# Kernel optimization log

Measured on AMD Instinct MI355X. Metric: run time of the kernel, lower is better.

The kernel has to match this reference:

```python
import jax, jax.numpy as jnp
import numpy as np

B, C, H = 2, 32, 64  # batch, concat channels, cube side (H==W==D required by attaxis reshapes)
Ch = C // 2


def _conv3d(x, w, b, pad):
    # conv3d block = Conv3d + bias + ReLU (n=1 conv block)
    y = jax.lax.conv_general_dilated(x, w, (1, 1, 1), [(p, p) for p in pad],
                                     dimension_numbers=('NCDHW', 'OIDHW', 'NCDHW'))
    return jax.nn.relu(y + b[None, :, None, None, None])


def setup_inputs():
    key = jax.random.key(0)
    ks = jax.random.split(key, 16)
    w = lambda k, s: jax.random.normal(k, s, dtype=jnp.float32) * 0.05
    z = lambda n: jnp.zeros((n,), jnp.float32)
    return {
        'x1': jax.random.normal(ks[0], (B, Ch, H, H, H), jnp.float32),
        'x2': jax.random.normal(ks[1], (B, Ch, H, H, H), jnp.float32),
        'w_red': w(ks[2], (1, C, 3, 3, 3)), 'b_red': z(1),
        'w_cx': w(ks[3], (1, 1, 1, 1, H)), 'b_cx': z(1),
        'w_cy': w(ks[4], (1, 1, 1, H, 1)), 'b_cy': z(1),
        'w_cz': w(ks[5], (1, 1, H, 1, 1)), 'b_cz': z(1),
        'w_sp1': w(ks[6], (1, 1, 1, 1, 1)), 'b_sp1': z(1),
        'w_sp3': w(ks[7], (1, 1, 3, 3, 3)), 'b_sp3': z(1),
        'w_sp5a': w(ks[8], (1, 1, 3, 3, 3)), 'b_sp5a': z(1),
        'w_sp5b': w(ks[9], (1, 1, 3, 3, 3)), 'b_sp5b': z(1),
        'w_fus': w(ks[10], (C, 1, 3, 3, 3)), 'b_fus': z(C),
        'w_c1': w(ks[11], (Ch, Ch, 3, 3, 3)), 'b_c1': z(Ch),
        'w_c2': w(ks[12], (Ch, Ch, 3, 3, 3)), 'b_c2': z(Ch),
    }


def _kernal(x, w_cx, b_cx, w_cy, b_cy, w_cz, b_cz,
            w_sp1, b_sp1, w_sp3, b_sp3, w_sp5a, b_sp5a, w_sp5b, b_sp5b):
    b, c, h, ww, d = x.shape
    # xyzaxis: axis-collapsing convs, then attaxis attention over S = h*w tokens
    q = _conv3d(x, w_cx, b_cx, (0, 0, 0))                        # [b,1,h,w,1]
    k = jnp.swapaxes(_conv3d(x, w_cy, b_cy, (0, 0, 0)), 3, 4)    # [b,1,h,d,1]
    v = jnp.swapaxes(_conv3d(x, w_cz, b_cz, (0, 0, 0)), 2, 4)    # [b,1,d,w,1]
    S = h * ww
    Q = q.reshape(b, S, 1)
    K = k.reshape(b, S, 1)
    V = v.reshape(b, S, 1)
    qk = jax.nn.softmax(jnp.einsum('bsc,btc->bst', Q, K), axis=-1)  # [b,S,S]
    xyz = jnp.einsum('bst,btc->bsc', qk, V).reshape(b, 1, h, ww, 1)
    # multi-branch convs + full-tensor att(sp1, sp3, sp5)
    sp1 = _conv3d(x, w_sp1, b_sp1, (0, 0, 0))
    sp3 = _conv3d(x, w_sp3, b_sp3, (1, 1, 1))
    sp5 = _conv3d(_conv3d(x, w_sp5a, b_sp5a, (1, 1, 1)), w_sp5b, b_sp5b, (1, 1, 1))
    attn = jnp.matmul(jax.nn.softmax(jnp.matmul(sp1, sp3), axis=-1), sp5)
    return xyz + attn + x  # xyz broadcasts over last dim


def reference(x1, x2, w_red, b_red, w_cx, b_cx, w_cy, b_cy, w_cz, b_cz,
              w_sp1, b_sp1, w_sp3, b_sp3, w_sp5a, b_sp5a, w_sp5b, b_sp5b,
              w_fus, b_fus, w_c1, b_c1, w_c2, b_c2):
    x = jnp.concatenate([x1, x2], axis=1)                 # [B,C,H,H,H]
    hx = _conv3d(x, w_red, b_red, (1, 1, 1))              # DenseSP.reducePool -> 1 channel
    hx = _kernal(hx, w_cx, b_cx, w_cy, b_cy, w_cz, b_cz,
                 w_sp1, b_sp1, w_sp3, b_sp3, w_sp5a, b_sp5a, w_sp5b, b_sp5b)
    sp = jax.nn.sigmoid(_conv3d(hx, w_fus, b_fus, (1, 1, 1)) + x)  # DenseSP output
    x = sp * x + x
    c = x.shape[1] // 2
    y1 = _conv3d(x[:, :c] + x1, w_c1, b_c1, (1, 1, 1))
    y2 = _conv3d(x[:, c:] + x2, w_c2, b_c2, (1, 1, 1))
    return (y1, y2)
```

## Files before the change

kernel.cpp:

```cpp
#include <hip/hip_runtime.h>

#define DEVFN static __device__ __forceinline__

constexpr int HHH = 262144;
constexpr int HH  = 4096;
constexpr int SP  = 20;

typedef __attribute__((ext_vector_type(8))) short short8;
typedef __attribute__((ext_vector_type(4))) float f32x4;

#define OFF_HX   ((size_t)0)
#define OFF_SP3  (OFF_HX   + 2*(size_t)HHH)
#define OFF_SP5A (OFF_SP3  + 2*(size_t)HHH)
#define OFF_SP5B (OFF_SP5A + 2*(size_t)HHH)
#define OFF_HXO  (OFF_SP5B + 2*(size_t)HHH)
#define OFF_Q    (OFF_HXO  + 2*(size_t)HHH)
#define OFF_K    (OFF_Q    + 2*(size_t)HH)
#define OFF_V    (OFF_K    + 2*(size_t)HH)
#define OFF_XYZ  (OFF_V    + 2*(size_t)HH)
#define OFF_KM   (OFF_XYZ  + 2*(size_t)HH)
#define OFF_Z    (OFF_KM   + 16)
#define OFF_WPRE (OFF_Z    + 32*(size_t)HHH)

DEVFN unsigned short f2bf(float f)
{
    unsigned u = __builtin_bit_cast(unsigned, f);
    u += 0x7fffu + ((u >> 16) & 1u);
    return (unsigned short)(u >> 16);
}

DEVFN void stage20(const float* __restrict__ src, float* __restrict__ tile,
                   int z0, int y0, int x0, int tid)
{
    for (int i = tid; i < 1800; i += 256) {
        int lz = i / 180;
        int r  = i - lz * 180;
        int ly = r / 18;
        int lx = r - ly * 18;
        int gz = z0 - 1 + lz, gy = y0 - 1 + ly, gx = x0 - 1 + lx;
        float v = 0.f;
        if ((unsigned)(gz | gy | gx) < 64u)
            v = src[(gz * 64 + gy) * 64 + gx];
        tile[(lz * 10 + ly) * SP + lx] = v;
    }
}

DEVFN void loadnb(const float* __restrict__ tile, int tz, int ty, int txg,
                  float4* pa, float2* pb)
{
#pragma unroll
    for (int dz = 0; dz < 3; ++dz) {
#pragma unroll
        for (int dy = 0; dy < 3; ++dy) {
            const float* row = &tile[((tz + dz) * 10 + (ty + dy)) * SP + txg * 4];
            pa[dz * 3 + dy] = *(const float4*)row;
            pb[dz * 3 + dy] = *(const float2*)(row + 4);
        }
    }
}

DEVFN float4 conv27r(const float4* pa, const float2* pb,
                     const float* __restrict__ wc, float4 acc)
{
#pragma unroll
    for (int t = 0; t < 9; ++t) {
        float w0 = wc[3 * t], w1 = wc[3 * t + 1], w2 = wc[3 * t + 2];
        float4 p = pa[t];
        float2 q = pb[t];
        acc.x = fmaf(p.x, w0, fmaf(p.y, w1, fmaf(p.z, w2, acc.x)));
        acc.y = fmaf(p.y, w0, fmaf(p.z, w1, fmaf(p.w, w2, acc.y)));
        acc.z = fmaf(p.z, w0, fmaf(p.w, w1, fmaf(q.x, w2, acc.z)));
        acc.w = fmaf(p.w, w0, fmaf(q.x, w1, fmaf(q.y, w2, acc.w)));
    }
    return acc;
}

__global__ __launch_bounds__(256) void k_wprep(
    const float* __restrict__ w1, const float* __restrict__ w2,
    unsigned short* __restrict__ wpre)
{
    int item = blockIdx.x * 256 + threadIdx.x;
    if (item >= 1792) return;
    int half = item / 896;
    int rem  = item - half * 896;
    int t = rem >> 6, lane = rem & 63;
    const float* w = half ? w2 : w1;
    int co = lane & 15, g = lane >> 4;
    int cihalf = g & 1, tapsel = g >> 1;
    int tap = 2 * t + tapsel;
    unsigned v[4] = {0u, 0u, 0u, 0u};
    if (tap < 27) {
#pragma unroll
        for (int p = 0; p < 4; ++p) {
            unsigned short lo = f2bf(w[(co * 16 + cihalf * 8 + 2 * p) * 27 + tap]);
            unsigned short hi = f2bf(w[(co * 16 + cihalf * 8 + 2 * p + 1) * 27 + tap]);
            v[p] = (unsigned)lo | ((unsigned)hi << 16);
        }
    }
    uint4 pk = {v[0], v[1], v[2], v[3]};
    ((uint4*)wpre)[item] = pk;
}

__global__ __launch_bounds__(256) void k_conv_red32(
    const float* __restrict__ x1, const float* __restrict__ x2,
    const float* __restrict__ w, const float* __restrict__ bias,
    float* __restrict__ hx)
{
    __shared__ __align__(16) float buf[3][2000];
    const int tid = threadIdx.x;
    const int tz = tid >> 5, ty = (tid >> 2) & 7, txg = tid & 3;
    const int bz = blockIdx.z;
    const int b = bz >> 3, z0 = (bz & 7) * 8;
    const int y0 = blockIdx.y * 8, x0 = blockIdx.x * 16;

    int gofs[8], lidx[8];
    bool inb[8], act[8];
#pragma unroll
    for (int k = 0; k < 8; ++k) {
        int i = tid + k * 256;
        act[k] = (i < 1800);
        inb[k] = false; gofs[k] = 0; lidx[k] = 0;
        if (act[k]) {
            int lz = i / 180, r = i - lz * 180, ly = r / 18, lx = r - ly * 18;
            lidx[k] = (lz * 10 + ly) * SP + lx;
            int gz = z0 - 1 + lz, gy = y0 - 1 + ly, gx = x0 - 1 + lx;
            if ((unsigned)(gz | gy | gx) < 64u) {
                inb[k] = true;
                gofs[k] = (gz * 64 + gy) * 64 + gx;
            }
        }
    }

#define LOADCH(c, rdst)                                                         \
    {                                                                           \
        const float* s_ = ((c) < 16 ? x1 : x2) + (size_t)(b * 16 + ((c) & 15)) * HHH; \
        _Pragma("unroll")                                                       \
        for (int k = 0; k < 8; ++k) rdst[k] = (act[k] && inb[k]) ? s_[gofs[k]] : 0.f; \
    }
#define STORECH(buf_, rsrc)                                                     \
    {                                                                           \
        _Pragma("unroll")                                                       \
        for (int k = 0; k < 8; ++k) if (act[k]) (buf_)[lidx[k]] = rsrc[k];      \
    }

    float rcur[8], rnext[8];
    LOADCH(0, rcur);
    STORECH(buf[0], rcur);
    LOADCH(1, rcur);
    __syncthreads();

    float4 acc = {0.f, 0.f, 0.f, 0.f};
    int cur = 0;
    for (int c = 0; c < 32; ++c) {
        if (c + 2 < 32) LOADCH(c + 2, rnext);
        const float* wc = w + c * 27;
        const float* tb = buf[cur];
#pragma unroll
        for (int dz = 0; dz < 3; ++dz) {
#pragma unroll
            for (int dy = 0; dy < 3; ++dy) {
                const float* row = &tb[((tz + dz) * 10 + (ty + dy)) * SP + txg * 4];
                float4 p = *(const float4*)row;
                float2 q = *(const float2*)(row + 4);
                const float* wr = wc + (dz * 3 + dy) * 3;
                float w0 = wr[0], w1 = wr[1], w2 = wr[2];
                acc.x = fmaf(p.x, w0, fmaf(p.y, w1, fmaf(p.z, w2, acc.x)));
                acc.y = fmaf(p.y, w0, fmaf(p.z, w1, fmaf(p.w, w2, acc.y)));
                acc.z = fmaf(p.z, w0, fmaf(p.w, w1, fmaf(q.x, w2, acc.z)));
                acc.w = fmaf(p.w, w0, fmaf(q.x, w1, fmaf(q.y, w2, acc.w)));
            }
        }
        int nxt = cur == 2 ? 0 : cur + 1;
        if (c + 1 < 32) {
            STORECH(buf[nxt], rcur);
#pragma unroll
            for (int k = 0; k < 8; ++k) rcur[k] = rnext[k];
        }
        cur = nxt;
        __syncthreads();
    }
#undef LOADCH
#undef STORECH

    float bv = bias[0];
    float4 o = {fmaxf(acc.x + bv, 0.f), fmaxf(acc.y + bv, 0.f),
                fmaxf(acc.z + bv, 0.f), fmaxf(acc.w + bv, 0.f)};
    size_t oidx = (size_t)b * HHH + ((size_t)(z0 + tz) * 64 + (y0 + ty)) * 64 + (x0 + txg * 4);
    *(float4*)&hx[oidx] = o;
}

__global__ __launch_bounds__(256) void k_conv1ch(
    const float* __restrict__ in, const float* __restrict__ w,
    const float* __restrict__ bias, float* __restrict__ outp)
{
    __shared__ __align__(16) float tile[2000];
    const int tid = threadIdx.x;
    const int tz = tid >> 5, ty = (tid >> 2) & 7, txg = tid & 3;
    const int b  = blockIdx.z >> 3;
    const int z0 = (blockIdx.z & 7) * 8, y0 = blockIdx.y * 8, x0 = blockIdx.x * 16;

    stage20(in + (size_t)b * HHH, tile, z0, y0, x0, tid);
    __syncthreads();
    float4 pa[9]; float2 pb[9];
    loadnb(tile, tz, ty, txg, pa, pb);
    float4 acc = {0.f, 0.f, 0.f, 0.f};
    acc = conv27r(pa, pb, w, acc);
    float bv = bias[0];
    float4 o = {fmaxf(acc.x + bv, 0.f), fmaxf(acc.y + bv, 0.f),
                fmaxf(acc.z + bv, 0.f), fmaxf(acc.w + bv, 0.f)};
    size_t oidx = (size_t)b * HHH + ((size_t)(z0 + tz) * 64 + (y0 + ty)) * 64 + (x0 + txg * 4);
    *(float4*)&outp[oidx] = o;
}

__global__ __launch_bounds__(256) void k_conv1ch_dual(
    const float* __restrict__ in,
    const float* __restrict__ wa, const float* __restrict__ ba, float* __restrict__ oa,
    const float* __restrict__ wb, const float* __restrict__ bb, float* __restrict__ ob)
{
    __shared__ __align__(16) float tile[2000];
    const int tid = threadIdx.x;
    const int tz = tid >> 5, ty = (tid >> 2) & 7, txg = tid & 3;
    const int b  = blockIdx.z >> 3;
    const int z0 = (blockIdx.z & 7) * 8, y0 = blockIdx.y * 8, x0 = blockIdx.x * 16;

    stage20(in + (size_t)b * HHH, tile, z0, y0, x0, tid);
    __syncthreads();
    float4 pa[9]; float2 pb[9];
    loadnb(tile, tz, ty, txg, pa, pb);
    float4 zero = {0.f, 0.f, 0.f, 0.f};
    float4 aA = conv27r(pa, pb, wa, zero);
    float4 aB = conv27r(pa, pb, wb, zero);
    float bva = ba[0], bvb = bb[0];
    float4 ra = {fmaxf(aA.x + bva, 0.f), fmaxf(aA.y + bva, 0.f),
                 fmaxf(aA.z + bva, 0.f), fmaxf(aA.w + bva, 0.f)};
    float4 rb = {fmaxf(aB.x + bvb, 0.f), fmaxf(aB.y + bvb, 0.f),
                 fmaxf(aB.z + bvb, 0.f), fmaxf(aB.w + bvb, 0.f)};
    size_t oidx = (size_t)b * HHH + ((size_t)(z0 + tz) * 64 + (y0 + ty)) * 64 + (x0 + txg * 4);
    *(float4*)&oa[oidx] = ra;
    *(float4*)&ob[oidx] = rb;
}

__global__ __launch_bounds__(256) void k_qk(
    const float* __restrict__ hx,
    const float* __restrict__ wq, const float* __restrict__ bq,
    const float* __restrict__ wk, const float* __restrict__ bk,
    float* __restrict__ Q, float* __restrict__ K)
{
    const int bi = blockIdx.x;
    const float* src = hx + (size_t)bi * HH;
    const int tid = threadIdx.x;
    const int j = tid >> 2, q = tid & 3;

    float a = 0.f;
    const float4* sv = (const float4*)(src + j * 64 + q * 16);
#pragma unroll
    for (int k = 0; k < 4; ++k) {
        float4 vv = sv[k];
        a = fmaf(vv.x, wq[q * 16 + k * 4 + 0], a);
        a = fmaf(vv.y, wq[q * 16 + k * 4 + 1], a);
        a = fmaf(vv.z, wq[q * 16 + k * 4 + 2], a);
        a = fmaf(vv.w, wq[q * 16 + k * 4 + 3], a);
    }
    a += __shfl_xor(a, 1); a += __shfl_xor(a, 2);

    float c = 0.f;
#pragma unroll
    for (int jj = 0; jj < 16; ++jj)
        c = fmaf(src[(q * 16 + jj) * 64 + j], wk[q * 16 + jj], c);
    c += __shfl_xor(c, 1); c += __shfl_xor(c, 2);

    if (q == 0) {
        Q[(size_t)bi * 64 + j] = fmaxf(a + bq[0], 0.f);
        K[(size_t)bi * 64 + j] = fmaxf(c + bk[0], 0.f);
    }
}

__global__ __launch_bounds__(256) void k_v(
    const float* __restrict__ hx, const float* __restrict__ wv,
    const float* __restrict__ bv, float* __restrict__ V)
{
    const int bt = blockIdx.x;
    const int b = bt >> 6, t = bt & 63;
    const int tid = threadIdx.x;
    const int j = tid >> 2, q = tid & 3;
    const float* src = hx + (size_t)b * HHH + (size_t)j * 64 + t;
    float a = 0.f;
#pragma unroll
    for (int k = 0; k < 16; ++k) {
        int i = q * 16 + k;
        a = fmaf(src[(size_t)i * HH], wv[i], a);
    }
    a += __shfl_xor(a, 1); a += __shfl_xor(a, 2);
    if (q == 0)
        V[(size_t)b * HH + t * 64 + j] = fmaxf(a + bv[0], 0.f);
}

__global__ void k_kmax(const float* __restrict__ K, float* __restrict__ kmax)
{
    __shared__ float red[256];
    int b = blockIdx.x;
    float m = -1e30f;
    for (int u = threadIdx.x; u < 4096; u += 256) m = fmaxf(m, K[b * 4096 + u]);
    red[threadIdx.x] = m;
    __syncthreads();
    for (int s = 128; s > 0; s >>= 1) {
        if (threadIdx.x < s) red[threadIdx.x] = fmaxf(red[threadIdx.x], red[threadIdx.x + s]);
        __syncthreads();
    }
    if (threadIdx.x == 0) kmax[b] = red[0];
}

__global__ __launch_bounds__(256) void k_xyz(
    const float* __restrict__ Q, const float* __restrict__ K,
    const float* __restrict__ V, const float* __restrict__ kmax,
    float* __restrict__ xyz)
{
    __shared__ float pden[4][64];
    __shared__ float pnum[4][64];
    const int b = blockIdx.y;
    const int chunk = blockIdx.x;
    const int lane = threadIdx.x & 63;
    const int wv = __builtin_amdgcn_readfirstlane(threadIdx.x >> 6);
    const int s = chunk * 64 + lane;
    const float qv = Q[b * 4096 + s];
    const float m = qv * kmax[b];
    const float* Kp = K + b * 4096 + wv * 1024;
    const float* Vp = V + b * 4096 + wv * 1024;
    float den = 0.f, num = 0.f;
#pragma unroll 4
    for (int u = 0; u < 1024; ++u) {
        float e = __expf(fmaf(qv, Kp[u], -m));
        den += e;
        num = fmaf(e, Vp[u], num);
    }
    pden[wv][lane] = den;
    pnum[wv][lane] = num;
    __syncthreads();
    if (threadIdx.x < 64) {
        float d = pden[0][lane] + pden[1][lane] + pden[2][lane] + pden[3][lane];
        float n = pnum[0][lane] + pnum[1][lane] + pnum[2][lane] + pnum[3][lane];
        xyz[b * 4096 + s] = n / d;
    }
}

DEVFN void mac16(const float4* __restrict__ base, int vb, float a, float* acc)
{
    float4 q0 = base[vb], q1 = base[vb + 1], q2 = base[vb + 2], q3 = base[vb + 3];
    float qq[16] = {q0.x, q0.y, q0.z, q0.w, q1.x, q1.y, q1.z, q1.w,
                    q2.x, q2.y, q2.z, q2.w, q3.x, q3.y, q3.z, q3.w};
#pragma unroll
    for (int k = 0; k < 16; ++k) acc[k] = fmaf(a, qq[k], acc[k]);
}

__global__ __launch_bounds__(256) void k_attn(
    const float* __restrict__ hx, const float* __restrict__ sp3,
    const float* __restrict__ sp5, const float* __restrict__ xyz,
    const float* __restrict__ w_sp1, const float* __restrict__ b_sp1,
    float* __restrict__ hxo)
{
    __shared__ __align__(16) float s1[64 * 65];
    __shared__ __align__(16) float s3[4096];
    __shared__ __align__(16) float s5[4096];
    const int tid = threadIdx.x;
    const int bi = blockIdx.x;
    const size_t off = (size_t)bi * HH;
    const float w1 = w_sp1[0], bb = b_sp1[0];
    for (int idx = tid; idx < 4096; idx += 256) {
        float hv = hx[off + idx];
        s1[(idx >> 6) * 65 + (idx & 63)] = fmaxf(fmaf(w1, hv, bb), 0.f);
        s3[idx] = sp3[off + idx];
        s5[idx] = sp5[off + idx];
    }
    __syncthreads();
    const int j = tid >> 2, g = tid & 3, t0 = g * 16;
    float m[16];
#pragma unroll
    for (int k = 0; k < 16; ++k) m[k] = 0.f;
    const float4* s3v = (const float4*)s3;
    for (int r = 0; r < 64; ++r) {
        float a = s1[j * 65 + r];
        mac16(s3v, r * 16 + (t0 >> 2), a, m);
    }
    float mx = m[0];
#pragma unroll
    for (int k = 1; k < 16; ++k) mx = fmaxf(mx, m[k]);
    mx = fmaxf(mx, __shfl_xor(mx, 1));
    mx = fmaxf(mx, __shfl_xor(mx, 2));
    float e[16];
    float sum = 0.f;
#pragma unroll
    for (int k = 0; k < 16; ++k) { e[k] = __expf(m[k] - mx); sum += e[k]; }
    sum += __shfl_xor(sum, 1);
    sum += __shfl_xor(sum, 2);
    const float inv = 1.f / sum;
    __syncthreads();
#pragma unroll
    for (int k = 0; k < 16; ++k) s1[j * 65 + t0 + k] = e[k] * inv;
    __syncthreads();
    float acc[16];
#pragma unroll
    for (int k = 0; k < 16; ++k) acc[k] = 0.f;
    const float4* s5v = (const float4*)s5;
    for (int r = 0; r < 64; ++r) {
        float a = s1[j * 65 + r];
        mac16(s5v, r * 16 + (t0 >> 2), a, acc);
    }
    const float xv = xyz[(size_t)(bi >> 6) * HH + (size_t)(bi & 63) * 64 + j];
    const size_t ob = off + (size_t)j * 64 + t0;
#pragma unroll
    for (int k = 0; k < 16; ++k)
        hxo[ob + k] = xv + acc[k] + hx[ob + k];
}

DEVFN float zcalc(float gg, float bf, float xv)
{
    float t = fmaxf(gg + bf, 0.f) + xv;
    float s = 1.f / (1.f + __expf(-t));
    return xv * (s + 2.f);
}

__global__ __launch_bounds__(256) void k_fuse_half(
    const float* __restrict__ hxo, const float* __restrict__ x1,
    const float* __restrict__ x2, const float* __restrict__ w_fus,
    const float* __restrict__ b_fus, unsigned short* __restrict__ Zb)
{
    __shared__ __align__(16) float tile[2000];
    const int tid = threadIdx.x;
    const int tz = tid >> 5, ty = (tid >> 2) & 7, txg = tid & 3;
    const int bz = blockIdx.z;
    const int zt = bz & 7, bh = bz >> 3;
    const int b = bh >> 1, half = bh & 1;
    const int z0 = zt * 8, y0 = blockIdx.y * 8, x0 = blockIdx.x * 16;

    stage20(hxo + (size_t)b * HHH, tile, z0, y0, x0, tid);
    __syncthreads();
    float4 pa[9]; float2 pb[9];
    loadnb(tile, tz, ty, txg, pa, pb);

    const size_t vox = ((size_t)(z0 + tz) * 64 + (y0 + ty)) * 64 + (x0 + txg * 4);
    const float* xbase = (half ? x2 : x1) + (size_t)(b * 16) * HHH + vox;
    const float* wbase = w_fus + (half * 16) * 27;
    const float* bbase = b_fus + half * 16;

    unsigned zp[4][8];
#pragma unroll
    for (int cc = 0; cc < 16; ++cc) {
        float4 zero = {0.f, 0.f, 0.f, 0.f};
        float4 g = conv27r(pa, pb, wbase + cc * 27, zero);
        float4 xv = *(const float4*)(xbase + (size_t)cc * HHH);
        float bf = bbase[cc];
        unsigned short z0v = f2bf(zcalc(g.x, bf, xv.x));
        unsigned short z1v = f2bf(zcalc(g.y, bf, xv.y));
        unsigned short z2v = f2bf(zcalc(g.z, bf, xv.z));
        unsigned short z3v = f2bf(zcalc(g.w, bf, xv.w));
        int p = cc >> 1;
        if ((cc & 1) == 0) {
            zp[0][p] = z0v; zp[1][p] = z1v; zp[2][p] = z2v; zp[3][p] = z3v;
        } else {
            zp[0][p] |= (unsigned)z0v << 16; zp[1][p] |= (unsigned)z1v << 16;
            zp[2][p] |= (unsigned)z2v << 16; zp[3][p] |= (unsigned)z3v << 16;
        }
    }
    unsigned short* zo = Zb + ((size_t)bh * HHH + vox) * 16;
#pragma unroll
    for (int v = 0; v < 4; ++v) {
        uint4 lo = {zp[v][0], zp[v][1], zp[v][2], zp[v][3]};
        uint4 hi = {zp[v][4], zp[v][5], zp[v][6], zp[v][7]};
        *(uint4*)(zo + v * 16)     = lo;
        *(uint4*)(zo + v * 16 + 8) = hi;
    }
}

__global__ __launch_bounds__(512) void k_convc_mfma(
    const unsigned short* __restrict__ Zb,
    const unsigned short* __restrict__ wpre,
    const float* __restrict__ b1, const float* __restrict__ b2,
    float* __restrict__ out)
{
    __shared__ __align__(16) unsigned short tile[1800 * 16];
    const int tid = threadIdx.x;
    const int lane = tid & 63;
    const int wvid = tid >> 6;
    const int bz = blockIdx.z;
    const int b = bz >> 4, half = (bz >> 3) & 1, z0 = (bz & 7) * 8;
    const int y0 = blockIdx.y * 8, x0 = blockIdx.x * 16;
    const float* bias = half ? b2 : b1;

    const int g = lane >> 4;
    const int cihalf = g & 1;
    const int tapsel = g >> 1;

    short8 wf[14];
    const short8* wp = (const short8*)wpre + (half * 14) * 64 + lane;
#pragma unroll
    for (int t = 0; t < 14; ++t) wf[t] = wp[t * 64];

    float bfrag[4];
#pragma unroll
    for (int r = 0; r < 4; ++r) bfrag[r] = bias[g * 4 + r];

    const unsigned short* zsrc = Zb + (size_t)(b * 2 + half) * HHH * 16;
    for (int i = tid; i < 3600; i += 512) {
        int pos = i >> 1, h = i & 1;
        int lz = pos / 180;
        int r2 = pos - lz * 180;
        int ly = r2 / 18, lx = r2 - ly * 18;
        int gz = z0 - 1 + lz, gy = y0 - 1 + ly, gx = x0 - 1 + lx;
        uint4 pk = {0u, 0u, 0u, 0u};
        if ((unsigned)(gz | gy | gx) < 64u) {
            size_t gvox = ((size_t)(gz * 64 + gy)) * 64 + gx;
            pk = *(const uint4*)(zsrc + gvox * 16 + h * 8);
        }
        *(uint4*)&tile[pos * 16 + h * 8] = pk;
    }
    __syncthreads();

    int offs[14];
#pragma unroll
    for (int t = 0; t < 14; ++t) {
        int tap = 2 * t + tapsel;
        int tcl = tap < 27 ? tap : 26;
        int dz = tcl / 9, rr = tcl - dz * 9;
        int dy = rr / 3, dx = rr - dy * 3;
        offs[t] = (((dz * 10 + dy) * 18 + dx + (lane & 15)) << 5) + (cihalf << 4);
    }

    const char* tb = (const char*)tile;
    for (int rr = 0; rr < 8; ++rr) {
        int rowid = wvid * 8 + rr;
        int zr = rowid >> 3, yr = rowid & 7;
        int rbase = ((zr * 10 + yr) * 18) << 5;
        f32x4 acc = {0.f, 0.f, 0.f, 0.f};
        f32x4 acc2 = {0.f, 0.f, 0.f, 0.f};
#pragma unroll
        for (int t = 0; t < 14; t += 2) {
            short8 bf0 = *(const short8*)(tb + (rbase + offs[t]));
            acc = __builtin_amdgcn_mfma_f32_16x16x32_bf16(wf[t], bf0, acc, 0, 0, 0);
            short8 bf1 = *(const short8*)(tb + (rbase + offs[t + 1]));
            acc2 = __builtin_amdgcn_mfma_f32_16x16x32_bf16(wf[t + 1], bf1, acc2, 0, 0, 0);
        }
        size_t vox = ((size_t)(z0 + zr) * 64 + (y0 + yr)) * 64 + x0 + (lane & 15);
        float* ob = out + (size_t)half * (2 * 16 * (size_t)HHH) + (size_t)(b * 16) * HHH + vox;
#pragma unroll
        for (int r = 0; r < 4; ++r) {
            float v = acc[r] + acc2[r] + bfrag[r];
            ob[(size_t)(g * 4 + r) * HHH] = fmaxf(v, 0.f);
        }
    }
}

extern "C" void kernel_launch(void* const* d_in, const int* in_sizes, int n_in,
                              void* d_out, int out_size, void* d_ws, size_t ws_size,
                              hipStream_t stream)
{
    const float* x1     = (const float*)d_in[0];
    const float* x2     = (const float*)d_in[1];
    const float* w_red  = (const float*)d_in[2];
    const float* b_red  = (const float*)d_in[3];
    const float* w_cx   = (const float*)d_in[4];
    const float* b_cx   = (const float*)d_in[5];
    const float* w_cy   = (const float*)d_in[6];
    const float* b_cy   = (const float*)d_in[7];
    const float* w_cz   = (const float*)d_in[8];
    const float* b_cz   = (const float*)d_in[9];
    const float* w_sp1  = (const float*)d_in[10];
    const float* b_sp1  = (const float*)d_in[11];
    const float* w_sp3  = (const float*)d_in[12];
    const float* b_sp3  = (const float*)d_in[13];
    const float* w_sp5a = (const float*)d_in[14];
    const float* b_sp5a = (const float*)d_in[15];
    const float* w_sp5b = (const float*)d_in[16];
    const float* b_sp5b = (const float*)d_in[17];
    const float* w_fus  = (const float*)d_in[18];
    const float* b_fus  = (const float*)d_in[19];
    const float* w_c1   = (const float*)d_in[20];
    const float* b_c1   = (const float*)d_in[21];
    const float* w_c2   = (const float*)d_in[22];
    const float* b_c2   = (const float*)d_in[23];

    float* ws  = (float*)d_ws;
    float* out = (float*)d_out;

    float* HX   = ws + OFF_HX;
    float* SP3  = ws + OFF_SP3;
    float* SP5A = ws + OFF_SP5A;
    float* SP5B = ws + OFF_SP5B;
    float* HXO  = ws + OFF_HXO;
    float* Qb   = ws + OFF_Q;
    float* Kb   = ws + OFF_K;
    float* Vb   = ws + OFF_V;
    float* XYZb = ws + OFF_XYZ;
    float* KM   = ws + OFF_KM;
    unsigned short* Zb   = (unsigned short*)(ws + OFF_Z);
    unsigned short* WPRE = (unsigned short*)(ws + OFF_WPRE);

    k_wprep    <<<7, 256, 0, stream>>>(w_c1, w_c2, WPRE);
    k_conv_red32<<<dim3(4, 8, 16), 256, 0, stream>>>(x1, x2, w_red, b_red, HX);
    k_conv1ch_dual<<<dim3(4, 8, 16), 256, 0, stream>>>(HX, w_sp3, b_sp3, SP3,
                                                       w_sp5a, b_sp5a, SP5A);
    k_conv1ch  <<<dim3(4, 8, 16), 256, 0, stream>>>(SP5A, w_sp5b, b_sp5b, SP5B);
    k_qk       <<<128, 256, 0, stream>>>(HX, w_cx, b_cx, w_cy, b_cy, Qb, Kb);
    k_v        <<<128, 256, 0, stream>>>(HX, w_cz, b_cz, Vb);
    k_kmax     <<<2, 256, 0, stream>>>(Kb, KM);
    k_xyz      <<<dim3(64, 2), 256, 0, stream>>>(Qb, Kb, Vb, KM, XYZb);
    k_attn     <<<128, 256, 0, stream>>>(HX, SP3, SP5B, XYZb, w_sp1, b_sp1, HXO);
    k_fuse_half<<<dim3(4, 8, 32), 256, 0, stream>>>(HXO, x1, x2, w_fus, b_fus, Zb);
    k_convc_mfma<<<dim3(4, 8, 32), 512, 0, stream>>>(Zb, WPRE, b_c1, b_c2, out);
}
```

Before: 205.1 us.

## Split reduction conv over channel groups with partial sums and separate reduce

The 32-channel reduction conv is split into four 8-channel groups, each launched as its own blocks, which quadruples the block count. Each group writes a partial sum into a scratch region that aliases the later SP3..HXO buffers. A new small kernel sums the four partials, adds the bias and applies ReLU. This is meant to fix low occupancy (128 blocks on a large GPU), in exchange for extra global traffic for the partials and one extra launch.

```diff
diff --git a/kernel.cpp b/kernel.cpp
--- a/kernel.cpp
+++ b/kernel.cpp
@@ -21,6 +21,7 @@
 #define OFF_KM   (OFF_XYZ  + 2*(size_t)HH)
 #define OFF_Z    (OFF_KM   + 16)
 #define OFF_WPRE (OFF_Z    + 32*(size_t)HHH)
+#define OFF_PART OFF_SP3
 
 DEVFN unsigned short f2bf(float f)
 {
@@ -101,17 +102,16 @@
     ((uint4*)wpre)[item] = pk;
 }
 
-__global__ __launch_bounds__(256) void k_conv_red32(
+__global__ __launch_bounds__(256) void k_conv_red8v(
     const float* __restrict__ x1, const float* __restrict__ x2,
-    const float* __restrict__ w, const float* __restrict__ bias,
-    float* __restrict__ hx)
-{
-    __shared__ __align__(16) float buf[3][2000];
+    const float* __restrict__ w, float* __restrict__ part)
+{
+    __shared__ __align__(16) float buf[2][2000];
     const int tid = threadIdx.x;
     const int tz = tid >> 5, ty = (tid >> 2) & 7, txg = tid & 3;
     const int bz = blockIdx.z;
-    const int b = bz >> 3, z0 = (bz & 7) * 8;
-    const int y0 = blockIdx.y * 8, x0 = blockIdx.x * 16;
+    const int b = bz >> 5, grp = (bz >> 3) & 3, zt = bz & 7;
+    const int z0 = zt * 8, y0 = blockIdx.y * 8, x0 = blockIdx.x * 16;
 
     int gofs[8], lidx[8];
     bool inb[8], act[8];
@@ -131,9 +131,12 @@
         }
     }
 
-#define LOADCH(c, rdst)                                                         \
+    const int c0 = grp * 8;
+    const float* srcb = (c0 < 16 ? x1 : x2) + (size_t)(b * 16 + (c0 & 15)) * HHH;
+
+#define LOADCH(cc, rdst)                                                        \
     {                                                                           \
-        const float* s_ = ((c) < 16 ? x1 : x2) + (size_t)(b * 16 + ((c) & 15)) * HHH; \
+        const float* s_ = srcb + (size_t)(cc) * HHH;                            \
         _Pragma("unroll")                                                       \
         for (int k = 0; k < 8; ++k) rdst[k] = (act[k] && inb[k]) ? s_[gofs[k]] : 0.f; \
     }
@@ -143,18 +146,18 @@
         for (int k = 0; k < 8; ++k) if (act[k]) (buf_)[lidx[k]] = rsrc[k];      \
     }
 
-    float rcur[8], rnext[8];
-    LOADCH(0, rcur);
-    STORECH(buf[0], rcur);
-    LOADCH(1, rcur);
+    float r0[8], r1[8];
+    LOADCH(0, r0);
+    STORECH(buf[0], r0);
+    LOADCH(1, r0);
     __syncthreads();
 
     float4 acc = {0.f, 0.f, 0.f, 0.f};
-    int cur = 0;
-    for (int c = 0; c < 32; ++c) {
-        if (c + 2 < 32) LOADCH(c + 2, rnext);
-        const float* wc = w + c * 27;
-        const float* tb = buf[cur];
+    const float* wg = w + c0 * 27;
+    for (int cc = 0; cc < 8; ++cc) {
+        if (cc + 2 < 8) LOADCH(cc + 2, r1);
+        const float* wc = wg + cc * 27;
+        const float* tb = buf[cc & 1];
 #pragma unroll
         for (int dz = 0; dz < 3; ++dz) {
 #pragma unroll
@@ -170,23 +173,39 @@
                 acc.w = fmaf(p.w, w0, fmaf(q.x, w1, fmaf(q.y, w2, acc.w)));
             }
         }
-        int nxt = cur == 2 ? 0 : cur + 1;
-        if (c + 1 < 32) {
-            STORECH(buf[nxt], rcur);
-#pragma unroll
-            for (int k = 0; k < 8; ++k) rcur[k] = rnext[k];
-        }
-        cur = nxt;
+        if (cc + 1 < 8) {
+            STORECH(buf[(cc + 1) & 1], r0);
+#pragma unroll
+            for (int k = 0; k < 8; ++k) r0[k] = r1[k];
+        }
         __syncthreads();
     }
 #undef LOADCH
 #undef STORECH
 
+    size_t vox = ((size_t)(z0 + tz) * 64 + (y0 + ty)) * 64 + (x0 + txg * 4);
+    *(float4*)&part[(size_t)(grp * 2 + b) * HHH + vox] = acc;
+}
+
+__global__ __launch_bounds__(256) void k_red_sum(
+    const float* __restrict__ part, const float* __restrict__ bias,
+    float* __restrict__ hx)
+{
+    int idx = blockIdx.x * 256 + threadIdx.x;
+    int b = idx >> 16;
+    int o = idx & 65535;
+    const float4* p = (const float4*)part;
+    float4 s0 = p[(size_t)(0 * 2 + b) * 65536 + o];
+    float4 s1 = p[(size_t)(1 * 2 + b) * 65536 + o];
+    float4 s2 = p[(size_t)(2 * 2 + b) * 65536 + o];
+    float4 s3 = p[(size_t)(3 * 2 + b) * 65536 + o];
     float bv = bias[0];
-    float4 o = {fmaxf(acc.x + bv, 0.f), fmaxf(acc.y + bv, 0.f),
-                fmaxf(acc.z + bv, 0.f), fmaxf(acc.w + bv, 0.f)};
-    size_t oidx = (size_t)b * HHH + ((size_t)(z0 + tz) * 64 + (y0 + ty)) * 64 + (x0 + txg * 4);
-    *(float4*)&hx[oidx] = o;
+    float4 r;
+    r.x = fmaxf(s0.x + s1.x + s2.x + s3.x + bv, 0.f);
+    r.y = fmaxf(s0.y + s1.y + s2.y + s3.y + bv, 0.f);
+    r.z = fmaxf(s0.z + s1.z + s2.z + s3.z + bv, 0.f);
+    r.w = fmaxf(s0.w + s1.w + s2.w + s3.w + bv, 0.f);
+    ((float4*)hx)[(size_t)b * 65536 + o] = r;
 }
 
 __global__ __launch_bounds__(256) void k_conv1ch(
@@ -591,11 +610,13 @@
     float* Vb   = ws + OFF_V;
     float* XYZb = ws + OFF_XYZ;
     float* KM   = ws + OFF_KM;
+    float* PART = ws + OFF_PART;
     unsigned short* Zb   = (unsigned short*)(ws + OFF_Z);
     unsigned short* WPRE = (unsigned short*)(ws + OFF_WPRE);
 
     k_wprep    <<<7, 256, 0, stream>>>(w_c1, w_c2, WPRE);
-    k_conv_red32<<<dim3(4, 8, 16), 256, 0, stream>>>(x1, x2, w_red, b_red, HX);
+    k_conv_red8v<<<dim3(4, 8, 64), 256, 0, stream>>>(x1, x2, w_red, PART);
+    k_red_sum  <<<512, 256, 0, stream>>>(PART, b_red, HX);
     k_conv1ch_dual<<<dim3(4, 8, 16), 256, 0, stream>>>(HX, w_sp3, b_sp3, SP3,
                                                        w_sp5a, b_sp5a, SP5A);
     k_conv1ch  <<<dim3(4, 8, 16), 256, 0, stream>>>(SP5A, w_sp5b, b_sp5b, SP5B);
```

Result: slower. 217.3 us (+5.9%).
